# Optimization experiments

Measured on AMD Instinct MI355X. Metric: run time of the kernel, lower is better.

The kernel has to match this reference:

```python
import jax, jax.numpy as jnp
import numpy as np

B, N, S, D = 16, 4096, 1024, 256
O1, O2 = 256, 128

def setup_inputs() -> dict:
    key = jax.random.key(0)
    ks = jax.random.split(key, 16)
    inp = {
        'xyz1': jax.random.normal(ks[0], (B, 3, N), jnp.float32),
        'xyz2': jax.random.normal(ks[1], (B, 3, S), jnp.float32),
        'points1': jax.random.normal(ks[2], (B, D, N), jnp.float32),
        'points2': jax.random.normal(ks[3], (B, D, S), jnp.float32),
        'W1': jax.random.normal(ks[4], (O1, D), jnp.float32) * 0.05,
        'b1': jax.random.normal(ks[5], (O1,), jnp.float32) * 0.05,
        'g1': jax.random.uniform(ks[6], (O1,), jnp.float32, 0.5, 1.5),
        'be1': jax.random.normal(ks[7], (O1,), jnp.float32) * 0.05,
        'm1': jax.random.normal(ks[8], (O1,), jnp.float32) * 0.05,
        'v1': jax.random.uniform(ks[9], (O1,), jnp.float32, 0.5, 1.5),
        'W2': jax.random.normal(ks[10], (O2, O1), jnp.float32) * 0.05,
        'b2': jax.random.normal(ks[11], (O2,), jnp.float32) * 0.05,
        'g2': jax.random.uniform(ks[12], (O2,), jnp.float32, 0.5, 1.5),
        'be2': jax.random.normal(ks[13], (O2,), jnp.float32) * 0.05,
        'm2': jax.random.normal(ks[14], (O2,), jnp.float32) * 0.05,
        'v2': jax.random.uniform(ks[15], (O2,), jnp.float32, 0.5, 1.5),
    }
    return inp

def _conv_bn_relu(x, W, b, g, be, m, v):
    # 1x1 Conv1d == per-point channel matmul, then inference BatchNorm, then ReLU
    y = jnp.einsum('oc,bcn->bon', W, x) + b[None, :, None]
    y = (y - m[None, :, None]) * (g * jax.lax.rsqrt(v + 1e-5))[None, :, None] + be[None, :, None]
    return jax.nn.relu(y)

def reference(xyz1, xyz2, points1, points2, W1, b1, g1, be1, m1, v1, W2, b2, g2, be2, m2, v2):
    x1 = jnp.transpose(xyz1, (0, 2, 1))   # [B,N,3]
    x2 = jnp.transpose(xyz2, (0, 2, 1))   # [B,S,3]
    p2 = jnp.transpose(points2, (0, 2, 1))  # [B,S,D]
    # squared pairwise distances [B,N,S]
    d = (jnp.sum(x1 * x1, -1, keepdims=True)
         + jnp.sum(x2 * x2, -1)[:, None, :]
         - 2.0 * jnp.einsum('bnc,bmc->bnm', x1, x2))
    # 3 nearest neighbors (smallest distances) instead of full sort
    negd, idx = jax.lax.top_k(-d, 3)      # [B,N,3]
    d3 = -negd
    recip = 1.0 / (d3 + 1e-8)
    w = recip / jnp.sum(recip, -1, keepdims=True)  # [B,N,3]
    gathered = jax.vmap(lambda p, i: p[i])(p2, idx)  # [B,N,3,D]
    interp = jnp.sum(gathered * w[..., None], axis=2)  # [B,N,D]
    new = jnp.transpose(interp, (0, 2, 1)) + points1   # [B,D,N]
    y = _conv_bn_relu(new, W1, b1, g1, be1, m1, v1)
    y = _conv_bn_relu(y, W2, b2, g2, be2, m2, v2)
    return y
```

## Files before the change

kernel.cpp:

```cpp
#include <hip/hip_runtime.h>
#include <hip/hip_bf16.h>

#define BB 16
#define NN 4096
#define SS 1024
#define DD 256
#define O1C 256
#define O2C 128
#define NT 128

typedef __attribute__((ext_vector_type(8))) short bf16x8;
typedef __attribute__((ext_vector_type(4))) float f32x4;
typedef __attribute__((ext_vector_type(2))) unsigned int u32x2;

static __device__ __forceinline__ unsigned short f2bf(float f) {
    union { float f; unsigned u; } v; v.f = f;
    unsigned r = (v.u + 0x7fffu + ((v.u >> 16) & 1u)) >> 16;
    return (unsigned short)r;
}

__global__ __launch_bounds__(256) void prep_kernel(
    const float* __restrict__ W1, const float* __restrict__ W2,
    const float* __restrict__ b1, const float* __restrict__ g1,
    const float* __restrict__ be1, const float* __restrict__ m1,
    const float* __restrict__ v1,
    const float* __restrict__ b2, const float* __restrict__ g2,
    const float* __restrict__ be2, const float* __restrict__ m2,
    const float* __restrict__ v2,
    unsigned short* __restrict__ W1b, unsigned short* __restrict__ W2b,
    float* __restrict__ sc1, float* __restrict__ sh1,
    float* __restrict__ sc2, float* __restrict__ sh2)
{
    int t = blockIdx.x * 256 + threadIdx.x;
    if (t < O1C * DD) W1b[t] = f2bf(W1[t]);
    int t2 = t - O1C * DD;
    if (t2 >= 0 && t2 < O2C * O1C) W2b[t2] = f2bf(W2[t2]);
    if (t < O1C) {
        float s = g1[t] / sqrtf(v1[t] + 1e-5f);
        sc1[t] = s;
        sh1[t] = (b1[t] - m1[t]) * s + be1[t];
    }
    if (t2 >= 0 && t2 < O2C) {
        float s = g2[t2] / sqrtf(v2[t2] + 1e-5f);
        sc2[t2] = s;
        sh2[t2] = (b2[t2] - m2[t2]) * s + be2[t2];
    }
}

__global__ __launch_bounds__(256) void knn3_kernel(
    const float* __restrict__ xyz1,
    const float* __restrict__ xyz2,
    int* __restrict__ idx_out,
    float* __restrict__ w_out)
{
    __shared__ float4 q[SS];
    __shared__ float  cd[256][3];
    __shared__ int    ci[256][3];

    const int b    = blockIdx.x >> 6;
    const int tile = blockIdx.x & 63;
    const int p    = threadIdx.x & 63;
    const int seg  = threadIdx.x >> 6;
    const int n    = tile * 64 + p;

    const float* x2 = xyz2 + (size_t)b * 3 * SS;
    for (int s = threadIdx.x; s < SS; s += 256) {
        float xx = x2[s], yy = x2[SS + s], zz = x2[2 * SS + s];
        q[s] = make_float4(xx, yy, zz, xx * xx + yy * yy + zz * zz);
    }
    __syncthreads();

    const float* x1 = xyz1 + (size_t)b * 3 * NN;
    const float px = x1[n], py = x1[NN + n], pz = x1[2 * NN + n];
    const float pn = px * px + py * py + pz * pz;

    const float FINF = 3.402823466e+38f;
    float d0 = FINF, d1 = FINF, d2 = FINF;
    int   i0 = 0,    i1 = 0,    i2 = 0;

    const int s0 = seg * (SS / 4);
    #pragma unroll 4
    for (int s = s0; s < s0 + SS / 4; ++s) {
        float4 v = q[s];
        float d = pn + v.w - 2.0f * (px * v.x + py * v.y + pz * v.z);
        if (d < d2) {
            if (d < d1) {
                if (d < d0) { d2 = d1; i2 = i1; d1 = d0; i1 = i0; d0 = d; i0 = s; }
                else        { d2 = d1; i2 = i1; d1 = d;  i1 = s; }
            } else          { d2 = d;  i2 = s; }
        }
    }
    cd[threadIdx.x][0] = d0; cd[threadIdx.x][1] = d1; cd[threadIdx.x][2] = d2;
    ci[threadIdx.x][0] = i0; ci[threadIdx.x][1] = i1; ci[threadIdx.x][2] = i2;
    __syncthreads();

    if (threadIdx.x < 64) {
        float m0 = cd[p][0], m1v = cd[p][1], m2v = cd[p][2];
        int   j0 = ci[p][0], j1 = ci[p][1], j2 = ci[p][2];
        #pragma unroll
        for (int qq = 1; qq < 4; ++qq) {
            const int t = qq * 64 + p;
            #pragma unroll
            for (int c = 0; c < 3; ++c) {
                float d = cd[t][c]; int i = ci[t][c];
                if (d < m2v) {
                    if (d < m1v) {
                        if (d < m0) { m2v = m1v; j2 = j1; m1v = m0; j1 = j0; m0 = d; j0 = i; }
                        else        { m2v = m1v; j2 = j1; m1v = d;  j1 = i; }
                    } else          { m2v = d;  j2 = i; }
                }
            }
        }
        float r0 = 1.0f / (m0 + 1e-8f);
        float r1 = 1.0f / (m1v + 1e-8f);
        float r2 = 1.0f / (m2v + 1e-8f);
        float rs = 1.0f / (r0 + r1 + r2);
        size_t base = ((size_t)b * NN + n) * 3;
        idx_out[base + 0] = j0;
        idx_out[base + 1] = j1;
        idx_out[base + 2] = j2;
        w_out[base + 0] = r0 * rs;
        w_out[base + 1] = r1 * rs;
        w_out[base + 2] = r2 * rs;
    }
}

__global__ __launch_bounds__(512) void fused_mfma_kernel(
    const float* __restrict__ points1,
    const float* __restrict__ points2,
    const int*   __restrict__ idx_in,
    const float* __restrict__ w_in,
    const unsigned short* __restrict__ W1b,
    const unsigned short* __restrict__ W2b,
    const float* __restrict__ sc1, const float* __restrict__ sh1,
    const float* __restrict__ sc2, const float* __restrict__ sh2,
    float* __restrict__ out)
{
    __shared__ unsigned short T[NT * DD];

    const int blk  = blockIdx.x;
    const int b    = blk >> 5;
    const int n0   = (blk & 31) * NT;
    const int tid  = threadIdx.x;
    const int lane = tid & 63;
    const int w    = tid >> 6;

    {
        const int p  = tid & 127;
        const int cg = tid >> 7;
        const int n  = n0 + p;
        const size_t ibase = ((size_t)b * NN + n) * 3;
        const int   gi0 = idx_in[ibase + 0];
        const int   gi1 = idx_in[ibase + 1];
        const int   gi2 = idx_in[ibase + 2];
        const float gw0 = w_in[ibase + 0];
        const float gw1 = w_in[ibase + 1];
        const float gw2 = w_in[ibase + 2];
        const float* p1 = points1 + (size_t)b * DD * NN + n;
        const float* p2 = points2 + (size_t)b * DD * SS;

        for (int cc = 0; cc < 8; ++cc) {
            const int c0 = (cg * 8 + cc) * 8;
            bf16x8 v8;
            #pragma unroll
            for (int k = 0; k < 8; ++k) {
                const int c = c0 + k;
                const float* row = p2 + (size_t)c * SS;
                float val = p1[(size_t)c * NN]
                          + gw0 * row[gi0] + gw1 * row[gi1] + gw2 * row[gi2];
                v8[k] = (short)f2bf(val);
            }
            const int byteoff = p * 512 + ((c0 * 2) ^ ((p & 7) << 4));
            *reinterpret_cast<bf16x8*>(reinterpret_cast<char*>(T) + byteoff) = v8;
        }
    }
    __syncthreads();

    const int r16 = lane & 15;
    const int kg  = lane >> 4;
    const int wo  = w >> 1;
    const int wn  = w & 1;

    f32x4 acc[4][4] = {};
    for (int ks = 0; ks < 8; ++ks) {
        const int kk = ks * 32;
        bf16x8 a[4], bf[4];
        #pragma unroll
        for (int m = 0; m < 4; ++m) {
            const int o = wo * 64 + m * 16 + r16;
            a[m] = *reinterpret_cast<const bf16x8*>(W1b + (size_t)o * DD + kk + kg * 8);
        }
        #pragma unroll
        for (int j = 0; j < 4; ++j) {
            const int nn = wn * 64 + j * 16 + r16;
            const int byteoff = nn * 512 + (((kk + kg * 8) * 2) ^ ((nn & 7) << 4));
            bf[j] = *reinterpret_cast<const bf16x8*>(reinterpret_cast<const char*>(T) + byteoff);
        }
        #pragma unroll
        for (int m = 0; m < 4; ++m)
            #pragma unroll
            for (int j = 0; j < 4; ++j)
                acc[m][j] = __builtin_amdgcn_mfma_f32_16x16x32_bf16(a[m], bf[j], acc[m][j], 0, 0, 0);
    }
    __syncthreads();

    #pragma unroll
    for (int m = 0; m < 4; ++m) {
        const int o0 = wo * 64 + m * 16 + kg * 4;
        const float4 s4 = *reinterpret_cast<const float4*>(sc1 + o0);
        const float4 h4 = *reinterpret_cast<const float4*>(sh1 + o0);
        #pragma unroll
        for (int j = 0; j < 4; ++j) {
            const int nn = wn * 64 + j * 16 + r16;
            float v0 = fmaxf(acc[m][j][0] * s4.x + h4.x, 0.0f);
            float v1 = fmaxf(acc[m][j][1] * s4.y + h4.y, 0.0f);
            float v2 = fmaxf(acc[m][j][2] * s4.z + h4.z, 0.0f);
            float v3 = fmaxf(acc[m][j][3] * s4.w + h4.w, 0.0f);
            u32x2 pk;
            pk[0] = (unsigned)f2bf(v0) | ((unsigned)f2bf(v1) << 16);
            pk[1] = (unsigned)f2bf(v2) | ((unsigned)f2bf(v3) << 16);
            const int byteoff = nn * 512 + ((o0 * 2) ^ ((nn & 7) << 4));
            *reinterpret_cast<u32x2*>(reinterpret_cast<char*>(T) + byteoff) = pk;
        }
    }
    __syncthreads();

    f32x4 acc2[2][4] = {};
    for (int ks = 0; ks < 8; ++ks) {
        const int kk = ks * 32;
        bf16x8 a[2], bf[4];
        #pragma unroll
        for (int m = 0; m < 2; ++m) {
            const int o = wo * 32 + m * 16 + r16;
            a[m] = *reinterpret_cast<const bf16x8*>(W2b + (size_t)o * O1C + kk + kg * 8);
        }
        #pragma unroll
        for (int j = 0; j < 4; ++j) {
            const int nn = wn * 64 + j * 16 + r16;
            const int byteoff = nn * 512 + (((kk + kg * 8) * 2) ^ ((nn & 7) << 4));
            bf[j] = *reinterpret_cast<const bf16x8*>(reinterpret_cast<const char*>(T) + byteoff);
        }
        #pragma unroll
        for (int m = 0; m < 2; ++m)
            #pragma unroll
            for (int j = 0; j < 4; ++j)
                acc2[m][j] = __builtin_amdgcn_mfma_f32_16x16x32_bf16(a[m], bf[j], acc2[m][j], 0, 0, 0);
    }

    #pragma unroll
    for (int m = 0; m < 2; ++m) {
        const int o0 = wo * 32 + m * 16 + kg * 4;
        const float4 s4 = *reinterpret_cast<const float4*>(sc2 + o0);
        const float4 h4 = *reinterpret_cast<const float4*>(sh2 + o0);
        #pragma unroll
        for (int j = 0; j < 4; ++j) {
            const int nn = wn * 64 + j * 16 + r16;
            const size_t obase = ((size_t)b * O2C + o0) * NN + n0 + nn;
            out[obase]            = fmaxf(acc2[m][j][0] * s4.x + h4.x, 0.0f);
            out[obase + NN]       = fmaxf(acc2[m][j][1] * s4.y + h4.y, 0.0f);
            out[obase + 2 * NN]   = fmaxf(acc2[m][j][2] * s4.z + h4.z, 0.0f);
            out[obase + 3 * NN]   = fmaxf(acc2[m][j][3] * s4.w + h4.w, 0.0f);
        }
    }
}

extern "C" void kernel_launch(void* const* d_in, const int* in_sizes, int n_in,
                              void* d_out, int out_size, void* d_ws, size_t ws_size,
                              hipStream_t stream) {
    const float* xyz1    = (const float*)d_in[0];
    const float* xyz2    = (const float*)d_in[1];
    const float* points1 = (const float*)d_in[2];
    const float* points2 = (const float*)d_in[3];
    const float* W1  = (const float*)d_in[4];
    const float* b1  = (const float*)d_in[5];
    const float* g1  = (const float*)d_in[6];
    const float* be1 = (const float*)d_in[7];
    const float* m1  = (const float*)d_in[8];
    const float* v1  = (const float*)d_in[9];
    const float* W2  = (const float*)d_in[10];
    const float* b2  = (const float*)d_in[11];
    const float* g2  = (const float*)d_in[12];
    const float* be2 = (const float*)d_in[13];
    const float* m2  = (const float*)d_in[14];
    const float* v2  = (const float*)d_in[15];

    float* out = (float*)d_out;

    char* ws = (char*)d_ws;
    int*            ws_idx = (int*)ws;
    float*          ws_w   = (float*)(ws + 786432);
    unsigned short* W1b    = (unsigned short*)(ws + 1572864);
    unsigned short* W2b    = (unsigned short*)(ws + 1703936);
    float*          sc1    = (float*)(ws + 1769472);
    float*          sh1    = (float*)(ws + 1770496);
    float*          sc2    = (float*)(ws + 1771520);
    float*          sh2    = (float*)(ws + 1772032);

    prep_kernel<<<dim3(384), dim3(256), 0, stream>>>(
        W1, W2, b1, g1, be1, m1, v1, b2, g2, be2, m2, v2,
        W1b, W2b, sc1, sh1, sc2, sh2);

    knn3_kernel<<<dim3(BB * (NN / 64)), dim3(256), 0, stream>>>(
        xyz1, xyz2, ws_idx, ws_w);

    fused_mfma_kernel<<<dim3(BB * (NN / NT)), dim3(512), 0, stream>>>(
        points1, points2, ws_idx, ws_w,
        W1b, W2b, sc1, sh1, sc2, sh2, out);
}
```

Measured before the change: 268.2 us.

## Transpose points2 to point-major for coalesced gathers; widen kNN search to 512 threads

Adds a transpose kernel that rewrites points2 from [B,D,S] to [B,S,D], so the interpolation gather in the fused MFMA kernel reads contiguous float4 rows per neighbor index. Before, each thread gathered scattered single floats across channel rows. The gather loop is also remapped: each wave handles 16 points and each lane covers 4 channels. Separately, the kNN kernel now uses 512 threads with 8 segments per query to raise parallelism. The costs are an extra kernel launch, a full pass over points2 through a workspace buffer, and reads of points1 that are now strided per lane.

```diff
diff --git a/kernel.cpp b/kernel.cpp
--- a/kernel.cpp
+++ b/kernel.cpp
@@ -47,15 +47,42 @@
     }
 }
 
-__global__ __launch_bounds__(256) void knn3_kernel(
+__global__ __launch_bounds__(256) void transpose_kernel(
+    const float* __restrict__ p2,
+    float* __restrict__ p2t)
+{
+    __shared__ float tile[64][65];
+    const int b  = blockIdx.x >> 6;
+    const int ct = (blockIdx.x >> 4) & 3;
+    const int st = blockIdx.x & 15;
+    const int c0 = ct * 64, s0 = st * 64;
+    const int cl = threadIdx.x >> 6;
+    const int sl = threadIdx.x & 63;
+
+    const float* src = p2 + ((size_t)b * DD + c0) * SS + s0;
+    #pragma unroll
+    for (int r = 0; r < 16; ++r) {
+        const int c = r * 4 + cl;
+        tile[c][sl] = src[(size_t)c * SS + sl];
+    }
+    __syncthreads();
+    float* dst = p2t + ((size_t)b * SS + s0) * DD + c0;
+    #pragma unroll
+    for (int r = 0; r < 16; ++r) {
+        const int s = r * 4 + cl;
+        dst[(size_t)s * DD + sl] = tile[sl][s];
+    }
+}
+
+__global__ __launch_bounds__(512) void knn3_kernel(
     const float* __restrict__ xyz1,
     const float* __restrict__ xyz2,
     int* __restrict__ idx_out,
     float* __restrict__ w_out)
 {
     __shared__ float4 q[SS];
-    __shared__ float  cd[256][3];
-    __shared__ int    ci[256][3];
+    __shared__ float  cd[512][3];
+    __shared__ int    ci[512][3];
 
     const int b    = blockIdx.x >> 6;
     const int tile = blockIdx.x & 63;
@@ -64,7 +91,7 @@
     const int n    = tile * 64 + p;
 
     const float* x2 = xyz2 + (size_t)b * 3 * SS;
-    for (int s = threadIdx.x; s < SS; s += 256) {
+    for (int s = threadIdx.x; s < SS; s += 512) {
         float xx = x2[s], yy = x2[SS + s], zz = x2[2 * SS + s];
         q[s] = make_float4(xx, yy, zz, xx * xx + yy * yy + zz * zz);
     }
@@ -78,9 +105,9 @@
     float d0 = FINF, d1 = FINF, d2 = FINF;
     int   i0 = 0,    i1 = 0,    i2 = 0;
 
-    const int s0 = seg * (SS / 4);
+    const int s0 = seg * (SS / 8);
     #pragma unroll 4
-    for (int s = s0; s < s0 + SS / 4; ++s) {
+    for (int s = s0; s < s0 + SS / 8; ++s) {
         float4 v = q[s];
         float d = pn + v.w - 2.0f * (px * v.x + py * v.y + pz * v.z);
         if (d < d2) {
@@ -98,7 +125,7 @@
         float m0 = cd[p][0], m1v = cd[p][1], m2v = cd[p][2];
         int   j0 = ci[p][0], j1 = ci[p][1], j2 = ci[p][2];
         #pragma unroll
-        for (int qq = 1; qq < 4; ++qq) {
+        for (int qq = 1; qq < 8; ++qq) {
             const int t = qq * 64 + p;
             #pragma unroll
             for (int c = 0; c < 3; ++c) {
@@ -127,7 +154,7 @@
 
 __global__ __launch_bounds__(512) void fused_mfma_kernel(
     const float* __restrict__ points1,
-    const float* __restrict__ points2,
+    const float* __restrict__ p2t,
     const int*   __restrict__ idx_in,
     const float* __restrict__ w_in,
     const unsigned short* __restrict__ W1b,
@@ -146,32 +173,31 @@
     const int w    = tid >> 6;
 
     {
-        const int p  = tid & 127;
-        const int cg = tid >> 7;
-        const int n  = n0 + p;
-        const size_t ibase = ((size_t)b * NN + n) * 3;
-        const int   gi0 = idx_in[ibase + 0];
-        const int   gi1 = idx_in[ibase + 1];
-        const int   gi2 = idx_in[ibase + 2];
-        const float gw0 = w_in[ibase + 0];
-        const float gw1 = w_in[ibase + 1];
-        const float gw2 = w_in[ibase + 2];
-        const float* p1 = points1 + (size_t)b * DD * NN + n;
-        const float* p2 = points2 + (size_t)b * DD * SS;
-
-        for (int cc = 0; cc < 8; ++cc) {
-            const int c0 = (cg * 8 + cc) * 8;
-            bf16x8 v8;
-            #pragma unroll
-            for (int k = 0; k < 8; ++k) {
-                const int c = c0 + k;
-                const float* row = p2 + (size_t)c * SS;
-                float val = p1[(size_t)c * NN]
-                          + gw0 * row[gi0] + gw1 * row[gi1] + gw2 * row[gi2];
-                v8[k] = (short)f2bf(val);
-            }
-            const int byteoff = p * 512 + ((c0 * 2) ^ ((p & 7) << 4));
-            *reinterpret_cast<bf16x8*>(reinterpret_cast<char*>(T) + byteoff) = v8;
+        const float* p2tb = p2t + (size_t)b * SS * DD;
+        const float* p1b  = points1 + (size_t)b * DD * NN;
+        #pragma unroll 2
+        for (int pp = 0; pp < 16; ++pp) {
+            const int p = w * 16 + pp;
+            const int n = n0 + p;
+            const size_t ibase = ((size_t)b * NN + n) * 3;
+            const int   gi0 = idx_in[ibase + 0];
+            const int   gi1 = idx_in[ibase + 1];
+            const int   gi2 = idx_in[ibase + 2];
+            const float gw0 = w_in[ibase + 0];
+            const float gw1 = w_in[ibase + 1];
+            const float gw2 = w_in[ibase + 2];
+            const float4 r0 = *reinterpret_cast<const float4*>(p2tb + (size_t)gi0 * DD + 4 * lane);
+            const float4 r1 = *reinterpret_cast<const float4*>(p2tb + (size_t)gi1 * DD + 4 * lane);
+            const float4 r2 = *reinterpret_cast<const float4*>(p2tb + (size_t)gi2 * DD + 4 * lane);
+            const float x0 = p1b[(size_t)(4 * lane + 0) * NN + n] + gw0 * r0.x + gw1 * r1.x + gw2 * r2.x;
+            const float x1 = p1b[(size_t)(4 * lane + 1) * NN + n] + gw0 * r0.y + gw1 * r1.y + gw2 * r2.y;
+            const float x2 = p1b[(size_t)(4 * lane + 2) * NN + n] + gw0 * r0.z + gw1 * r1.z + gw2 * r2.z;
+            const float x3 = p1b[(size_t)(4 * lane + 3) * NN + n] + gw0 * r0.w + gw1 * r1.w + gw2 * r2.w;
+            u32x2 pk;
+            pk[0] = (unsigned)f2bf(x0) | ((unsigned)f2bf(x1) << 16);
+            pk[1] = (unsigned)f2bf(x2) | ((unsigned)f2bf(x3) << 16);
+            const int byteoff = p * 512 + ((8 * lane) ^ ((p & 7) << 4));
+            *reinterpret_cast<u32x2*>(reinterpret_cast<char*>(T) + byteoff) = pk;
         }
     }
     __syncthreads();
@@ -295,15 +321,18 @@
     float*          sh1    = (float*)(ws + 1770496);
     float*          sc2    = (float*)(ws + 1771520);
     float*          sh2    = (float*)(ws + 1772032);
+    float*          p2t    = (float*)(ws + 2097152);
 
     prep_kernel<<<dim3(384), dim3(256), 0, stream>>>(
         W1, W2, b1, g1, be1, m1, v1, b2, g2, be2, m2, v2,
         W1b, W2b, sc1, sh1, sc2, sh2);
 
-    knn3_kernel<<<dim3(BB * (NN / 64)), dim3(256), 0, stream>>>(
+    transpose_kernel<<<dim3(BB * 64), dim3(256), 0, stream>>>(points2, p2t);
+
+    knn3_kernel<<<dim3(BB * (NN / 64)), dim3(512), 0, stream>>>(
         xyz1, xyz2, ws_idx, ws_w);
 
     fused_mfma_kernel<<<dim3(BB * (NN / NT)), dim3(512), 0, stream>>>(
-        points1, points2, ws_idx, ws_w,
+        points1, p2t, ws_idx, ws_w,
         W1b, W2b, sc1, sh1, sc2, sh2, out);
 }
```

Measured after the change: 276.8 us. +3.2%, slower.
